# Optimization experiments

Measured on AMD Instinct MI355X. Metric: run time of the kernel, lower is better.

Reference implementation:

```python
import jax, jax.numpy as jnp
import numpy as np

N_NODES = 50000
E0, E1 = 500000, 300000
D = 64  # node_embedding_size == h_feats == edge_embedding_sizes[i]


def _mlp(x, w0, b0, w1, b1, w2, b2):
    # Linear -> ReLU -> Linear -> ReLU -> Linear (nodes_in / edges_in stacks)
    h = jax.nn.relu(x @ w0 + b0)
    h = jax.nn.relu(h @ w1 + b1)
    return h @ w2 + b2


def setup_inputs() -> dict:
    key = jax.random.key(0)
    ks = jax.random.split(key, 32)

    def lin(k, fi, fo):
        return (jax.random.uniform(k, (fi, fo), jnp.float32) - 0.5) * (2.0 / np.sqrt(fi))

    z = lambda n: jnp.zeros((n,), jnp.float32)
    inp = {}
    inp['node_feats'] = jax.random.normal(ks[0], (N_NODES, 32), jnp.float32)
    inp['edge_feats0'] = jax.random.normal(ks[1], (E0, 16), jnp.float32)
    inp['edge_feats1'] = jax.random.normal(ks[2], (E1, 8), jnp.float32)
    # nodes_in MLP
    inp['n_w0'], inp['n_b0'] = lin(ks[3], 32, D), z(D)
    inp['n_w1'], inp['n_b1'] = lin(ks[4], D, D), z(D)
    inp['n_w2'], inp['n_b2'] = lin(ks[5], D, D), z(D)
    # edges_in MLP for edge type 0 (16 -> 64)
    inp['e0_w0'], inp['e0_b0'] = lin(ks[6], 16, D), z(D)
    inp['e0_w1'], inp['e0_b1'] = lin(ks[7], D, D), z(D)
    inp['e0_w2'], inp['e0_b2'] = lin(ks[8], D, D), z(D)
    # edges_in MLP for edge type 1 (8 -> 64)
    inp['e1_w0'], inp['e1_b0'] = lin(ks[9], 8, D), z(D)
    inp['e1_w1'], inp['e1_b1'] = lin(ks[10], D, D), z(D)
    inp['e1_w2'], inp['e1_b2'] = lin(ks[11], D, D), z(D)
    # GraphConv weights
    inp['c1_w'], inp['c1_b'] = lin(ks[12], D, D), z(D)
    inp['c2_w'], inp['c2_b'] = lin(ks[13], D, 1), z(1)
    # edge list (type-0 edges first, then type-1 edges)
    inp['src'] = jax.random.randint(ks[14], (E0 + E1,), 0, N_NODES, dtype=jnp.int32)
    inp['dst'] = jax.random.randint(ks[15], (E0 + E1,), 0, N_NODES, dtype=jnp.int32)
    return inp


def reference(node_feats, edge_feats0, edge_feats1,
              n_w0, n_b0, n_w1, n_b1, n_w2, n_b2,
              e0_w0, e0_b0, e0_w1, e0_b1, e0_w2, e0_b2,
              e1_w0, e1_b0, e1_w1, e1_b1, e1_w2, e1_b2,
              c1_w, c1_b, c2_w, c2_b, src, dst):
    n = node_feats.shape[0]
    # dense embedding stacks
    hn = _mlp(node_feats, n_w0, n_b0, n_w1, n_b1, n_w2, n_b2)          # [N, D]
    he = jnp.concatenate([
        _mlp(edge_feats0, e0_w0, e0_b0, e0_w1, e0_b1, e0_w2, e0_b2),
        _mlp(edge_feats1, e1_w0, e1_b0, e1_w1, e1_b1, e1_w2, e1_b2),
    ], axis=0)                                                          # [E, D]
    # GraphConv symmetric normalization (DGL norm='both'), degrees clamped to 1
    ones = jnp.ones(src.shape, jnp.float32)
    deg_out = jnp.maximum(jax.ops.segment_sum(ones, src, num_segments=n), 1.0)
    deg_in = jnp.maximum(jax.ops.segment_sum(ones, dst, num_segments=n), 1.0)
    norm_e = jax.lax.rsqrt(deg_out[src] * deg_in[dst])[:, None]        # [E, 1]
    # conv1: u_add_v message plus edge embedding, normalized sum aggregation
    msg = (hn[src] + hn[dst] + he) * norm_e                            # [E, D]
    agg1 = jax.ops.segment_sum(msg, dst, num_segments=n)               # [N, D]
    h1 = jax.nn.relu(agg1 @ c1_w + c1_b)                               # [N, D]
    # conv2: standard GraphConv to scalar output
    agg2 = jax.ops.segment_sum(h1[src] * norm_e, dst, num_segments=n)  # [N, D]
    return agg2 @ c2_w + c2_b                                          # [N, 1]
```

## Files before the change

### kernel.cpp

```cpp
#include <hip/hip_runtime.h>

#define N_NODES 50000
#define NE0 500000
#define NE1 300000
#define NE (NE0 + NE1)
#define DD 64
#define ILV 9

typedef __bf16 bf16x8 __attribute__((ext_vector_type(8)));
typedef float f32x4 __attribute__((ext_vector_type(4)));
typedef unsigned short u16x8 __attribute__((ext_vector_type(8)));

__device__ __forceinline__ ushort f2bf(float x) {
  union { __bf16 h; ushort u; } v;
  v.h = (__bf16)x;
  return v.u;
}
__device__ __forceinline__ float bf2f(ushort u) {
  union { unsigned u; float f; } v;
  v.u = ((unsigned)u) << 16;
  return v.f;
}

__global__ void pack_k(const float* __restrict__ w00, const float* __restrict__ w01,
                       const float* __restrict__ w02, const float* __restrict__ w10,
                       const float* __restrict__ w11, const float* __restrict__ w12,
                       const float* __restrict__ w20, const float* __restrict__ w21,
                       const float* __restrict__ w22, ushort* __restrict__ pk) {
  int f = blockIdx.x, l = threadIdx.x;
  int t = f / 20, fl = f % 20;
  int layer, nt, ks;
  if (fl < 4) { layer = 0; nt = fl; ks = 0; }
  else if (fl < 12) { layer = 1; nt = (fl - 4) >> 1; ks = (fl - 4) & 1; }
  else { layer = 2; nt = (fl - 12) >> 1; ks = (fl - 12) & 1; }
  const float* Wt[3][3] = {{w00, w01, w02}, {w10, w11, w12}, {w20, w21, w22}};
  const int K0[3] = {16, 8, 32};
  const float* W = Wt[t][layer];
  int K = (layer == 0) ? K0[t] : 64;
  int g = l >> 4, c = l & 15;
  ushort o[8];
#pragma unroll
  for (int e = 0; e < 8; ++e) {
    int k = ks * 32 + g * 8 + e, n = nt * 16 + c;
    o[e] = f2bf((k < K) ? W[k * DD + n] : 0.f);
  }
  ushort4* d4 = (ushort4*)&pk[(size_t)f * 512 + l * 8];
  d4[0] = make_ushort4(o[0], o[1], o[2], o[3]);
  d4[1] = make_ushort4(o[4], o[5], o[6], o[7]);
}

__device__ __forceinline__ int block_scan_excl(int x, int tid, int* total) {
  int lane = tid & 63, w = tid >> 6;
  int incl = x;
#pragma unroll
  for (int d = 1; d < 64; d <<= 1) {
    int y = __shfl_up(incl, d);
    if (lane >= d) incl += y;
  }
  __shared__ int wsum[4];
  if (lane == 63) wsum[w] = incl;
  __syncthreads();
  int woff = 0;
  if (w > 0) woff = wsum[0];
  if (w > 1) woff += wsum[1];
  if (w > 2) woff += wsum[2];
  *total = wsum[0] + wsum[1] + wsum[2] + wsum[3];
  return woff + incl - x;
}

__global__ __launch_bounds__(256) void scan_k(const int* __restrict__ cnt,
                                              int* __restrict__ rowptr,
                                              int* __restrict__ gbase) {
  int i = blockIdx.x * 256 + threadIdx.x;
  int x = (i < N_NODES) ? cnt[i] : 0;
  int tot;
  int ex = block_scan_excl(x, threadIdx.x, &tot);
  __shared__ int base;
  if (threadIdx.x == 0) base = atomicAdd(gbase, tot);
  __syncthreads();
  if (i < N_NODES) rowptr[i] = base + ex;
}

__global__ void scatter_k(const int* __restrict__ src, const int* __restrict__ dst,
                          const int* __restrict__ rowptr,
                          const int* __restrict__ rank,
                          const int* __restrict__ cntO,
                          const int* __restrict__ cntI,
                          int4* __restrict__ cslot) {
  int e = blockIdx.x * 256 + threadIdx.x;
  if (e < NE) {
    int s = src[e], d = dst[e];
    int slot = rowptr[d] + rank[e];
    float nm = rsqrtf((float)max(cntO[s], 1) * (float)max(cntI[d], 1));
    int4 q;
    q.x = e;
    q.y = s;
    q.z = __float_as_int(nm);
    q.w = 0;
    cslot[slot] = q;
  }
}

template <int FIN, bool NODE>
__device__ __forceinline__ void mlp_body(
    ushort (*__restrict__ A)[72], const float* __restrict__ xin,
    const ushort* __restrict__ pk, int pkb, const float* __restrict__ B0,
    const float* __restrict__ B1, const float* __restrict__ B2,
    ushort* __restrict__ msg, float* __restrict__ hn, int r0w, int nR,
    int ebase) {
  const int l = threadIdx.x & 63;
  const int g = l >> 4, c = l & 15;

  {
    int row = l >> 1, half = l & 1;
    int r = r0w + row;
    bool ok = r < nR;
    if (FIN == 32) {
      int cq = half * 16;
#pragma unroll
      for (int q = 0; q < 4; ++q) {
        float4 v = make_float4(0.f, 0.f, 0.f, 0.f);
        if (ok) v = *(const float4*)(xin + (size_t)r * 32 + cq + q * 4);
        *(ushort4*)&A[row][cq + q * 4] =
            make_ushort4(f2bf(v.x), f2bf(v.y), f2bf(v.z), f2bf(v.w));
      }
    } else if (FIN == 16) {
      int cq = half * 8;
#pragma unroll
      for (int q = 0; q < 2; ++q) {
        float4 v = make_float4(0.f, 0.f, 0.f, 0.f);
        if (ok) v = *(const float4*)(xin + (size_t)r * 16 + cq + q * 4);
        *(ushort4*)&A[row][cq + q * 4] =
            make_ushort4(f2bf(v.x), f2bf(v.y), f2bf(v.z), f2bf(v.w));
      }
    } else {
      int cq = half * 4;
      float4 v = make_float4(0.f, 0.f, 0.f, 0.f);
      if (ok) v = *(const float4*)(xin + (size_t)r * 8 + cq);
      *(ushort4*)&A[row][cq] =
          make_ushort4(f2bf(v.x), f2bf(v.y), f2bf(v.z), f2bf(v.w));
    }
  }
  asm volatile("s_waitcnt lgkmcnt(0)" ::: "memory");

  f32x4 acc[2][4];
#pragma unroll
  for (int nt = 0; nt < 4; ++nt) {
    float b = B0[nt * 16 + c];
    acc[0][nt] = f32x4{b, b, b, b};
    acc[1][nt] = acc[0][nt];
  }
  {
    bf16x8 a0 = {}, a1 = {};
    if (g * 8 < FIN) {
      a0 = *(const bf16x8*)&A[c][g * 8];
      a1 = *(const bf16x8*)&A[16 + c][g * 8];
    }
#pragma unroll
    for (int nt = 0; nt < 4; ++nt) {
      bf16x8 bb = *(const bf16x8*)&pk[(size_t)(pkb + nt) * 512 + l * 8];
      acc[0][nt] = __builtin_amdgcn_mfma_f32_16x16x32_bf16(a0, bb, acc[0][nt], 0, 0, 0);
      acc[1][nt] = __builtin_amdgcn_mfma_f32_16x16x32_bf16(a1, bb, acc[1][nt], 0, 0, 0);
    }
  }
#pragma unroll
  for (int t = 0; t < 2; ++t)
#pragma unroll
    for (int nt = 0; nt < 4; ++nt)
#pragma unroll
      for (int r = 0; r < 4; ++r)
        A[t * 16 + g * 4 + r][nt * 16 + c] = f2bf(fmaxf(acc[t][nt][r], 0.f));
  asm volatile("s_waitcnt lgkmcnt(0)" ::: "memory");

#pragma unroll
  for (int nt = 0; nt < 4; ++nt) {
    float b = B1[nt * 16 + c];
    acc[0][nt] = f32x4{b, b, b, b};
    acc[1][nt] = acc[0][nt];
  }
  {
    bf16x8 x00 = *(const bf16x8*)&A[c][g * 8];
    bf16x8 x01 = *(const bf16x8*)&A[c][32 + g * 8];
    bf16x8 x10 = *(const bf16x8*)&A[16 + c][g * 8];
    bf16x8 x11 = *(const bf16x8*)&A[16 + c][32 + g * 8];
#pragma unroll
    for (int nt = 0; nt < 4; ++nt) {
      bf16x8 bb0 = *(const bf16x8*)&pk[(size_t)(pkb + 4 + nt * 2) * 512 + l * 8];
      bf16x8 bb1 = *(const bf16x8*)&pk[(size_t)(pkb + 5 + nt * 2) * 512 + l * 8];
      acc[0][nt] = __builtin_amdgcn_mfma_f32_16x16x32_bf16(x00, bb0, acc[0][nt], 0, 0, 0);
      acc[0][nt] = __builtin_amdgcn_mfma_f32_16x16x32_bf16(x01, bb1, acc[0][nt], 0, 0, 0);
      acc[1][nt] = __builtin_amdgcn_mfma_f32_16x16x32_bf16(x10, bb0, acc[1][nt], 0, 0, 0);
      acc[1][nt] = __builtin_amdgcn_mfma_f32_16x16x32_bf16(x11, bb1, acc[1][nt], 0, 0, 0);
    }
  }
#pragma unroll
  for (int t = 0; t < 2; ++t)
#pragma unroll
    for (int nt = 0; nt < 4; ++nt)
#pragma unroll
      for (int r = 0; r < 4; ++r)
        A[t * 16 + g * 4 + r][nt * 16 + c] = f2bf(fmaxf(acc[t][nt][r], 0.f));
  asm volatile("s_waitcnt lgkmcnt(0)" ::: "memory");

#pragma unroll
  for (int nt = 0; nt < 4; ++nt) {
    float b = B2[nt * 16 + c];
    acc[0][nt] = f32x4{b, b, b, b};
    acc[1][nt] = acc[0][nt];
  }
  {
    bf16x8 x00 = *(const bf16x8*)&A[c][g * 8];
    bf16x8 x01 = *(const bf16x8*)&A[c][32 + g * 8];
    bf16x8 x10 = *(const bf16x8*)&A[16 + c][g * 8];
    bf16x8 x11 = *(const bf16x8*)&A[16 + c][32 + g * 8];
#pragma unroll
    for (int nt = 0; nt < 4; ++nt) {
      bf16x8 bb0 = *(const bf16x8*)&pk[(size_t)(pkb + 12 + nt * 2) * 512 + l * 8];
      bf16x8 bb1 = *(const bf16x8*)&pk[(size_t)(pkb + 13 + nt * 2) * 512 + l * 8];
      acc[0][nt] = __builtin_amdgcn_mfma_f32_16x16x32_bf16(x00, bb0, acc[0][nt], 0, 0, 0);
      acc[0][nt] = __builtin_amdgcn_mfma_f32_16x16x32_bf16(x01, bb1, acc[0][nt], 0, 0, 0);
      acc[1][nt] = __builtin_amdgcn_mfma_f32_16x16x32_bf16(x10, bb0, acc[1][nt], 0, 0, 0);
      acc[1][nt] = __builtin_amdgcn_mfma_f32_16x16x32_bf16(x11, bb1, acc[1][nt], 0, 0, 0);
    }
  }

  if (NODE) {
#pragma unroll
    for (int t = 0; t < 2; ++t)
#pragma unroll
      for (int r = 0; r < 4; ++r) {
        int n = r0w + t * 16 + g * 4 + r;
        if (n < nR) {
          float* hp = hn + (size_t)n * DD + c;
#pragma unroll
          for (int nt = 0; nt < 4; ++nt) hp[nt * 16] = acc[t][nt][r];
        }
      }
  } else {
#pragma unroll
    for (int t = 0; t < 2; ++t)
#pragma unroll
      for (int nt = 0; nt < 4; ++nt)
#pragma unroll
        for (int r = 0; r < 4; ++r)
          A[t * 16 + g * 4 + r][nt * 16 + c] = f2bf(acc[t][nt][r]);
    asm volatile("s_waitcnt lgkmcnt(0)" ::: "memory");
#pragma unroll
    for (int p = 0; p < 4; ++p) {
      int row = p * 8 + (l >> 3);
      int col8 = (l & 7) * 8;
      u16x8 v = *(const u16x8*)&A[row][col8];
      if (r0w + row < nR)
        *(u16x8*)(msg + (size_t)(ebase + r0w + row) * DD + col8) = v;
    }
  }
}

__global__ __launch_bounds__(256, 6) void giant_k(
    const float* __restrict__ nf, const float* __restrict__ ef0,
    const float* __restrict__ ef1, const ushort* __restrict__ pk,
    const float* __restrict__ nb0, const float* __restrict__ nb1,
    const float* __restrict__ nb2, const float* __restrict__ b00,
    const float* __restrict__ b01, const float* __restrict__ b02,
    const float* __restrict__ b10, const float* __restrict__ b11,
    const float* __restrict__ b12, const int* __restrict__ src,
    const int* __restrict__ dst, int* __restrict__ cntO,
    int* __restrict__ cntI, int* __restrict__ rank,
    ushort* __restrict__ msg, float* __restrict__ hn,
    int NBc4, int NBn, int NB0v, int NB1v) {
  __shared__ __align__(16) ushort act[4][32][72];
  int bid = blockIdx.x, tid = threadIdx.x, wid = tid >> 6;
  int cnum = bid / ILV;
  if (bid % ILV == ILV - 1) {
    if (cnum < NBc4) {
      int t4 = (cnum * 256 + tid) * 4;
      if (t4 < NE) {
        int4 s4 = *(const int4*)(src + t4);
        int4 d4 = *(const int4*)(dst + t4);
        atomicAdd(cntO + s4.x, 1);
        atomicAdd(cntO + s4.y, 1);
        atomicAdd(cntO + s4.z, 1);
        atomicAdd(cntO + s4.w, 1);
        int4 r;
        r.x = atomicAdd(cntI + d4.x, 1);
        r.y = atomicAdd(cntI + d4.y, 1);
        r.z = atomicAdd(cntI + d4.z, 1);
        r.w = atomicAdd(cntI + d4.w, 1);
        *(int4*)(rank + t4) = r;
      }
    }
    return;
  }
  int mb = bid - cnum;
  if (mb >= NBn + NB0v + NB1v) return;
  ushort (*A)[72] = act[wid];
  if (mb < NBn) {
    mlp_body<32, true>(A, nf, pk, 40, nb0, nb1, nb2, nullptr, hn,
                       mb * 128 + wid * 32, N_NODES, 0);
  } else if (mb < NBn + NB0v) {
    mlp_body<16, false>(A, ef0, pk, 0, b00, b01, b02, msg, nullptr,
                        (mb - NBn) * 128 + wid * 32, NE0, 0);
  } else {
    mlp_body<8, false>(A, ef1, pk, 20, b10, b11, b12, msg, nullptr,
                       (mb - NBn - NB0v) * 128 + wid * 32, NE1, NE0);
  }
}

__global__ __launch_bounds__(256) void gather_conv1_k(
    const int* __restrict__ rowptr, const int* __restrict__ deg,
    const int4* __restrict__ cslot, const ushort* __restrict__ msgb,
    const float* __restrict__ hn, const float* __restrict__ c1w,
    const float* __restrict__ c1b, const float* __restrict__ c2w,
    float* __restrict__ sbuf) {
  int w = threadIdx.x >> 6, l = threadIdx.x & 63;
  int g = l >> 4, c = l & 15;
  int n = blockIdx.x * 4 + w;
  if (n >= N_NODES) return;
  int r0 = rowptr[n], r1 = r0 + deg[n];
  float a0 = 0.f, a1 = 0.f, a2 = 0.f, a3 = 0.f, sn = 0.f;
  for (int j0 = r0; j0 < r1; j0 += 16) {
#pragma unroll
    for (int u = 0; u < 4; ++u) {
      int j = j0 + u * 4 + g;
      bool v = j < r1;
      int js = v ? j : r0;
      int4 q = cslot[js];
      int e = q.x, s = q.y;
      float nm = v ? __int_as_float(q.z) : 0.f;
      ushort4 m = *(const ushort4*)(msgb + (size_t)e * DD + c * 4);
      float4 h = *(const float4*)(hn + (size_t)s * DD + c * 4);
      a0 = fmaf(nm, bf2f(m.x) + h.x, a0);
      a1 = fmaf(nm, bf2f(m.y) + h.y, a1);
      a2 = fmaf(nm, bf2f(m.z) + h.z, a2);
      a3 = fmaf(nm, bf2f(m.w) + h.w, a3);
      sn += nm;
    }
  }
  a0 += __shfl_xor(a0, 16); a0 += __shfl_xor(a0, 32);
  a1 += __shfl_xor(a1, 16); a1 += __shfl_xor(a1, 32);
  a2 += __shfl_xor(a2, 16); a2 += __shfl_xor(a2, 32);
  a3 += __shfl_xor(a3, 16); a3 += __shfl_xor(a3, 32);
  sn += __shfl_xor(sn, 16); sn += __shfl_xor(sn, 32);
  float4 hv = *(const float4*)(hn + (size_t)n * DD + c * 4);
  a0 = fmaf(sn, hv.x, a0);
  a1 = fmaf(sn, hv.y, a1);
  a2 = fmaf(sn, hv.z, a2);
  a3 = fmaf(sn, hv.w, a3);
  __shared__ float Asm[4][64];
  if (g == 0) *(float4*)&Asm[w][c * 4] = make_float4(a0, a1, a2, a3);
  float h = c1b[l];
#pragma unroll 8
  for (int k = 0; k < 64; ++k) h = fmaf(Asm[w][k], c1w[k * DD + l], h);
  h = fmaxf(h, 0.f);
  float v = h * c2w[l];
#pragma unroll
  for (int d = 32; d; d >>= 1) v += __shfl_xor(v, d);
  if (l == 0) sbuf[n] = v;
}

__global__ __launch_bounds__(256) void conv2_gather_k(
    const int* __restrict__ rowptr, const int* __restrict__ deg,
    const int4* __restrict__ cslot, const float* __restrict__ sbuf,
    const float* __restrict__ c2b, float* __restrict__ out) {
  int n = blockIdx.x * 16 + (threadIdx.x >> 4);
  int c = threadIdx.x & 15;
  if (n >= N_NODES) return;
  int r0 = rowptr[n], r1 = r0 + deg[n];
  float a = 0.f;
  for (int j = r0 + c; j < r1; j += 16) {
    int4 q = cslot[j];
    a = fmaf(__int_as_float(q.z), sbuf[q.y], a);
  }
  a += __shfl_xor(a, 1, 16);
  a += __shfl_xor(a, 2, 16);
  a += __shfl_xor(a, 4, 16);
  a += __shfl_xor(a, 8, 16);
  if (c == 0) out[n] = a + c2b[0];
}

extern "C" void kernel_launch(void* const* d_in, const int* in_sizes, int n_in,
                              void* d_out, int out_size, void* d_ws,
                              size_t ws_size, hipStream_t stream) {
  const float* nf   = (const float*)d_in[0];
  const float* ef0  = (const float*)d_in[1];
  const float* ef1  = (const float*)d_in[2];
  const float* n_w0 = (const float*)d_in[3];  const float* n_b0 = (const float*)d_in[4];
  const float* n_w1 = (const float*)d_in[5];  const float* n_b1 = (const float*)d_in[6];
  const float* n_w2 = (const float*)d_in[7];  const float* n_b2 = (const float*)d_in[8];
  const float* e0w0 = (const float*)d_in[9];  const float* e0b0 = (const float*)d_in[10];
  const float* e0w1 = (const float*)d_in[11]; const float* e0b1 = (const float*)d_in[12];
  const float* e0w2 = (const float*)d_in[13]; const float* e0b2 = (const float*)d_in[14];
  const float* e1w0 = (const float*)d_in[15]; const float* e1b0 = (const float*)d_in[16];
  const float* e1w1 = (const float*)d_in[17]; const float* e1b1 = (const float*)d_in[18];
  const float* e1w2 = (const float*)d_in[19]; const float* e1b2 = (const float*)d_in[20];
  const float* c1w  = (const float*)d_in[21]; const float* c1b  = (const float*)d_in[22];
  const float* c2w  = (const float*)d_in[23]; const float* c2b  = (const float*)d_in[24];
  const int* src = (const int*)d_in[25];
  const int* dst = (const int*)d_in[26];
  float* out = (float*)d_out;
  float* ws = (float*)d_ws;

  float*  hn     = ws;
  float*  sbuf   = ws + 3200000;
  int*    rowptr = (int*)(ws + 3250000);
  int*    cntI   = (int*)(ws + 3300008);
  int*    cntO   = (int*)(ws + 3350008);
  int*    gbase  = (int*)(ws + 3400008);
  int*    rank   = (int*)(ws + 3410000);
  int4*   cslot  = (int4*)(ws + 4210000);
  ushort* msg    = (ushort*)(ws + 7410000);
  ushort* pk     = (ushort*)(ws + 33010000);

  const int NB   = (N_NODES + 255) / 256;
  const int NBn  = (N_NODES + 127) / 128;
  const int NB0  = (NE0 + 127) / 128;
  const int NB1  = (NE1 + 127) / 128;
  const int NBc  = (NE + 255) / 256;
  const int NBc4 = (NE + 1023) / 1024;

  const int NMLP = NBn + NB0 + NB1;
  int T = NMLP + NBc4;
  while (T / ILV < NBc4 || T - T / ILV < NMLP) ++T;

  hipMemsetAsync(cntI, 0, (size_t)100016 * sizeof(int), stream);
  pack_k<<<60, 64, 0, stream>>>(e0w0, e0w1, e0w2, e1w0, e1w1, e1w2, n_w0,
                                n_w1, n_w2, pk);
  giant_k<<<T, 256, 0, stream>>>(
      nf, ef0, ef1, pk, n_b0, n_b1, n_b2, e0b0, e0b1, e0b2, e1b0, e1b1, e1b2,
      src, dst, cntO, cntI, rank, msg, hn, NBc4, NBn, NB0, NB1);
  scan_k<<<NB, 256, 0, stream>>>(cntI, rowptr, gbase);
  scatter_k<<<NBc, 256, 0, stream>>>(src, dst, rowptr, rank, cntO, cntI,
                                     cslot);
  gather_conv1_k<<<(N_NODES + 3) / 4, 256, 0, stream>>>(
      rowptr, cntI, cslot, msg, hn, c1w, c1b, c2w, sbuf);
  conv2_gather_k<<<(N_NODES + 15) / 16, 256, 0, stream>>>(
      rowptr, cntI, cslot, sbuf, c2b, out);
}
```

Measured before the change: 196.2 us.

## Fuse edge MLPs into per-node gather, dropping the bf16 edge message buffer

The edge-embedding MLP is no longer computed up front and written to a bf16 message buffer. It now runs inside the per-node gather kernel on 16-edge tiles read through the CSR slots, with the normalized results accumulated directly. In-degree counts are split by edge type so each node's type-0 and type-1 edges sit contiguously in CSR order and can use the matching MLP weights. The counting kernel now interleaves only the node MLP with the edge counting. This removes roughly 100MB of message write and reread traffic, but adds gathered, uncoalesced reads of edge features and partially filled MFMA tiles for low-degree nodes, which wastes MFMA work.

```diff
diff --git a/kernel.cpp b/kernel.cpp
--- a/kernel.cpp
+++ b/kernel.cpp
@@ -5,21 +5,14 @@
 #define NE1 300000
 #define NE (NE0 + NE1)
 #define DD 64
-#define ILV 9
 
 typedef __bf16 bf16x8 __attribute__((ext_vector_type(8)));
 typedef float f32x4 __attribute__((ext_vector_type(4)));
-typedef unsigned short u16x8 __attribute__((ext_vector_type(8)));
 
 __device__ __forceinline__ ushort f2bf(float x) {
   union { __bf16 h; ushort u; } v;
   v.h = (__bf16)x;
   return v.u;
-}
-__device__ __forceinline__ float bf2f(ushort u) {
-  union { unsigned u; float f; } v;
-  v.u = ((unsigned)u) << 16;
-  return v.f;
 }
 
 __global__ void pack_k(const float* __restrict__ w00, const float* __restrict__ w01,
@@ -68,11 +61,12 @@
   return woff + incl - x;
 }
 
-__global__ __launch_bounds__(256) void scan_k(const int* __restrict__ cnt,
+__global__ __launch_bounds__(256) void scan_k(const int* __restrict__ cntI0,
+                                              const int* __restrict__ cntI1,
                                               int* __restrict__ rowptr,
                                               int* __restrict__ gbase) {
   int i = blockIdx.x * 256 + threadIdx.x;
-  int x = (i < N_NODES) ? cnt[i] : 0;
+  int x = (i < N_NODES) ? (cntI0[i] + cntI1[i]) : 0;
   int tot;
   int ex = block_scan_excl(x, threadIdx.x, &tot);
   __shared__ int base;
@@ -85,13 +79,15 @@
                           const int* __restrict__ rowptr,
                           const int* __restrict__ rank,
                           const int* __restrict__ cntO,
-                          const int* __restrict__ cntI,
+                          const int* __restrict__ cntI0,
+                          const int* __restrict__ cntI1,
                           int4* __restrict__ cslot) {
   int e = blockIdx.x * 256 + threadIdx.x;
   if (e < NE) {
     int s = src[e], d = dst[e];
-    int slot = rowptr[d] + rank[e];
-    float nm = rsqrtf((float)max(cntO[s], 1) * (float)max(cntI[d], 1));
+    int slot = rowptr[d] + ((e < NE0) ? rank[e] : cntI0[d] + rank[e]);
+    float nm = rsqrtf((float)max(cntO[s], 1) *
+                      (float)max(cntI0[d] + cntI1[d], 1));
     int4 q;
     q.x = e;
     q.y = s;
@@ -101,48 +97,27 @@
   }
 }
 
-template <int FIN, bool NODE>
-__device__ __forceinline__ void mlp_body(
-    ushort (*__restrict__ A)[72], const float* __restrict__ xin,
-    const ushort* __restrict__ pk, int pkb, const float* __restrict__ B0,
+__device__ __forceinline__ void node_body(
+    ushort (*__restrict__ A)[72], const float* __restrict__ nf,
+    const ushort* __restrict__ pk, const float* __restrict__ B0,
     const float* __restrict__ B1, const float* __restrict__ B2,
-    ushort* __restrict__ msg, float* __restrict__ hn, int r0w, int nR,
-    int ebase) {
+    float* __restrict__ hn, int r0w) {
   const int l = threadIdx.x & 63;
   const int g = l >> 4, c = l & 15;
-
   {
     int row = l >> 1, half = l & 1;
     int r = r0w + row;
-    bool ok = r < nR;
-    if (FIN == 32) {
-      int cq = half * 16;
-#pragma unroll
-      for (int q = 0; q < 4; ++q) {
-        float4 v = make_float4(0.f, 0.f, 0.f, 0.f);
-        if (ok) v = *(const float4*)(xin + (size_t)r * 32 + cq + q * 4);
-        *(ushort4*)&A[row][cq + q * 4] =
-            make_ushort4(f2bf(v.x), f2bf(v.y), f2bf(v.z), f2bf(v.w));
-      }
-    } else if (FIN == 16) {
-      int cq = half * 8;
-#pragma unroll
-      for (int q = 0; q < 2; ++q) {
-        float4 v = make_float4(0.f, 0.f, 0.f, 0.f);
-        if (ok) v = *(const float4*)(xin + (size_t)r * 16 + cq + q * 4);
-        *(ushort4*)&A[row][cq + q * 4] =
-            make_ushort4(f2bf(v.x), f2bf(v.y), f2bf(v.z), f2bf(v.w));
-      }
-    } else {
-      int cq = half * 4;
+    bool ok = r < N_NODES;
+    int cq = half * 16;
+#pragma unroll
+    for (int q = 0; q < 4; ++q) {
       float4 v = make_float4(0.f, 0.f, 0.f, 0.f);
-      if (ok) v = *(const float4*)(xin + (size_t)r * 8 + cq);
-      *(ushort4*)&A[row][cq] =
+      if (ok) v = *(const float4*)(nf + (size_t)r * 32 + cq + q * 4);
+      *(ushort4*)&A[row][cq + q * 4] =
           make_ushort4(f2bf(v.x), f2bf(v.y), f2bf(v.z), f2bf(v.w));
     }
   }
   asm volatile("s_waitcnt lgkmcnt(0)" ::: "memory");
-
   f32x4 acc[2][4];
 #pragma unroll
   for (int nt = 0; nt < 4; ++nt) {
@@ -151,14 +126,11 @@
     acc[1][nt] = acc[0][nt];
   }
   {
-    bf16x8 a0 = {}, a1 = {};
-    if (g * 8 < FIN) {
-      a0 = *(const bf16x8*)&A[c][g * 8];
-      a1 = *(const bf16x8*)&A[16 + c][g * 8];
-    }
+    bf16x8 a0 = *(const bf16x8*)&A[c][g * 8];
+    bf16x8 a1 = *(const bf16x8*)&A[16 + c][g * 8];
 #pragma unroll
     for (int nt = 0; nt < 4; ++nt) {
-      bf16x8 bb = *(const bf16x8*)&pk[(size_t)(pkb + nt) * 512 + l * 8];
+      bf16x8 bb = *(const bf16x8*)&pk[(size_t)(40 + nt) * 512 + l * 8];
       acc[0][nt] = __builtin_amdgcn_mfma_f32_16x16x32_bf16(a0, bb, acc[0][nt], 0, 0, 0);
       acc[1][nt] = __builtin_amdgcn_mfma_f32_16x16x32_bf16(a1, bb, acc[1][nt], 0, 0, 0);
     }
@@ -171,109 +143,66 @@
       for (int r = 0; r < 4; ++r)
         A[t * 16 + g * 4 + r][nt * 16 + c] = f2bf(fmaxf(acc[t][nt][r], 0.f));
   asm volatile("s_waitcnt lgkmcnt(0)" ::: "memory");
-
-#pragma unroll
-  for (int nt = 0; nt < 4; ++nt) {
-    float b = B1[nt * 16 + c];
-    acc[0][nt] = f32x4{b, b, b, b};
-    acc[1][nt] = acc[0][nt];
-  }
-  {
+#pragma unroll
+  for (int L = 0; L < 2; ++L) {
+    const float* B = L ? B2 : B1;
+    int pb = L ? 52 : 44;
+#pragma unroll
+    for (int nt = 0; nt < 4; ++nt) {
+      float b = B[nt * 16 + c];
+      acc[0][nt] = f32x4{b, b, b, b};
+      acc[1][nt] = acc[0][nt];
+    }
     bf16x8 x00 = *(const bf16x8*)&A[c][g * 8];
     bf16x8 x01 = *(const bf16x8*)&A[c][32 + g * 8];
     bf16x8 x10 = *(const bf16x8*)&A[16 + c][g * 8];
     bf16x8 x11 = *(const bf16x8*)&A[16 + c][32 + g * 8];
 #pragma unroll
     for (int nt = 0; nt < 4; ++nt) {
-      bf16x8 bb0 = *(const bf16x8*)&pk[(size_t)(pkb + 4 + nt * 2) * 512 + l * 8];
-      bf16x8 bb1 = *(const bf16x8*)&pk[(size_t)(pkb + 5 + nt * 2) * 512 + l * 8];
+      bf16x8 bb0 = *(const bf16x8*)&pk[(size_t)(pb + nt * 2) * 512 + l * 8];
+      bf16x8 bb1 = *(const bf16x8*)&pk[(size_t)(pb + 1 + nt * 2) * 512 + l * 8];
       acc[0][nt] = __builtin_amdgcn_mfma_f32_16x16x32_bf16(x00, bb0, acc[0][nt], 0, 0, 0);
       acc[0][nt] = __builtin_amdgcn_mfma_f32_16x16x32_bf16(x01, bb1, acc[0][nt], 0, 0, 0);
       acc[1][nt] = __builtin_amdgcn_mfma_f32_16x16x32_bf16(x10, bb0, acc[1][nt], 0, 0, 0);
       acc[1][nt] = __builtin_amdgcn_mfma_f32_16x16x32_bf16(x11, bb1, acc[1][nt], 0, 0, 0);
     }
+    if (L == 0) {
+#pragma unroll
+      for (int t = 0; t < 2; ++t)
+#pragma unroll
+        for (int nt = 0; nt < 4; ++nt)
+#pragma unroll
+          for (int r = 0; r < 4; ++r)
+            A[t * 16 + g * 4 + r][nt * 16 + c] = f2bf(fmaxf(acc[t][nt][r], 0.f));
+      asm volatile("s_waitcnt lgkmcnt(0)" ::: "memory");
+    }
   }
 #pragma unroll
   for (int t = 0; t < 2; ++t)
 #pragma unroll
-    for (int nt = 0; nt < 4; ++nt)
-#pragma unroll
-      for (int r = 0; r < 4; ++r)
-        A[t * 16 + g * 4 + r][nt * 16 + c] = f2bf(fmaxf(acc[t][nt][r], 0.f));
-  asm volatile("s_waitcnt lgkmcnt(0)" ::: "memory");
-
-#pragma unroll
-  for (int nt = 0; nt < 4; ++nt) {
-    float b = B2[nt * 16 + c];
-    acc[0][nt] = f32x4{b, b, b, b};
-    acc[1][nt] = acc[0][nt];
-  }
-  {
-    bf16x8 x00 = *(const bf16x8*)&A[c][g * 8];
-    bf16x8 x01 = *(const bf16x8*)&A[c][32 + g * 8];
-    bf16x8 x10 = *(const bf16x8*)&A[16 + c][g * 8];
-    bf16x8 x11 = *(const bf16x8*)&A[16 + c][32 + g * 8];
-#pragma unroll
-    for (int nt = 0; nt < 4; ++nt) {
-      bf16x8 bb0 = *(const bf16x8*)&pk[(size_t)(pkb + 12 + nt * 2) * 512 + l * 8];
-      bf16x8 bb1 = *(const bf16x8*)&pk[(size_t)(pkb + 13 + nt * 2) * 512 + l * 8];
-      acc[0][nt] = __builtin_amdgcn_mfma_f32_16x16x32_bf16(x00, bb0, acc[0][nt], 0, 0, 0);
-      acc[0][nt] = __builtin_amdgcn_mfma_f32_16x16x32_bf16(x01, bb1, acc[0][nt], 0, 0, 0);
-      acc[1][nt] = __builtin_amdgcn_mfma_f32_16x16x32_bf16(x10, bb0, acc[1][nt], 0, 0, 0);
-      acc[1][nt] = __builtin_amdgcn_mfma_f32_16x16x32_bf16(x11, bb1, acc[1][nt], 0, 0, 0);
-    }
-  }
-
-  if (NODE) {
-#pragma unroll
-    for (int t = 0; t < 2; ++t)
-#pragma unroll
-      for (int r = 0; r < 4; ++r) {
-        int n = r0w + t * 16 + g * 4 + r;
-        if (n < nR) {
-          float* hp = hn + (size_t)n * DD + c;
-#pragma unroll
-          for (int nt = 0; nt < 4; ++nt) hp[nt * 16] = acc[t][nt][r];
-        }
+    for (int r = 0; r < 4; ++r) {
+      int n = r0w + t * 16 + g * 4 + r;
+      if (n < N_NODES) {
+        float* hp = hn + (size_t)n * DD + c;
+#pragma unroll
+        for (int nt = 0; nt < 4; ++nt) hp[nt * 16] = acc[t][nt][r];
       }
-  } else {
-#pragma unroll
-    for (int t = 0; t < 2; ++t)
-#pragma unroll
-      for (int nt = 0; nt < 4; ++nt)
-#pragma unroll
-        for (int r = 0; r < 4; ++r)
-          A[t * 16 + g * 4 + r][nt * 16 + c] = f2bf(acc[t][nt][r]);
-    asm volatile("s_waitcnt lgkmcnt(0)" ::: "memory");
-#pragma unroll
-    for (int p = 0; p < 4; ++p) {
-      int row = p * 8 + (l >> 3);
-      int col8 = (l & 7) * 8;
-      u16x8 v = *(const u16x8*)&A[row][col8];
-      if (r0w + row < nR)
-        *(u16x8*)(msg + (size_t)(ebase + r0w + row) * DD + col8) = v;
-    }
-  }
-}
-
-__global__ __launch_bounds__(256, 6) void giant_k(
-    const float* __restrict__ nf, const float* __restrict__ ef0,
-    const float* __restrict__ ef1, const ushort* __restrict__ pk,
+    }
+}
+
+__global__ __launch_bounds__(256, 6) void countnode_k(
+    const float* __restrict__ nf, const ushort* __restrict__ pk,
     const float* __restrict__ nb0, const float* __restrict__ nb1,
-    const float* __restrict__ nb2, const float* __restrict__ b00,
-    const float* __restrict__ b01, const float* __restrict__ b02,
-    const float* __restrict__ b10, const float* __restrict__ b11,
-    const float* __restrict__ b12, const int* __restrict__ src,
+    const float* __restrict__ nb2, const int* __restrict__ src,
     const int* __restrict__ dst, int* __restrict__ cntO,
-    int* __restrict__ cntI, int* __restrict__ rank,
-    ushort* __restrict__ msg, float* __restrict__ hn,
-    int NBc4, int NBn, int NB0v, int NB1v) {
+    int* __restrict__ cntI0, int* __restrict__ cntI1,
+    int* __restrict__ rank, float* __restrict__ hn, int NBc4, int NBn) {
   __shared__ __align__(16) ushort act[4][32][72];
   int bid = blockIdx.x, tid = threadIdx.x, wid = tid >> 6;
-  int cnum = bid / ILV;
-  if (bid % ILV == ILV - 1) {
-    if (cnum < NBc4) {
-      int t4 = (cnum * 256 + tid) * 4;
+  if (bid % 3 != 2) {
+    int cidx = (bid / 3) * 2 + (bid % 3);
+    if (cidx < NBc4) {
+      int t4 = (cidx * 256 + tid) * 4;
       if (t4 < NE) {
         int4 s4 = *(const int4*)(src + t4);
         int4 d4 = *(const int4*)(dst + t4);
@@ -281,58 +210,155 @@
         atomicAdd(cntO + s4.y, 1);
         atomicAdd(cntO + s4.z, 1);
         atomicAdd(cntO + s4.w, 1);
+        int* cI = (t4 < NE0) ? cntI0 : cntI1;
         int4 r;
-        r.x = atomicAdd(cntI + d4.x, 1);
-        r.y = atomicAdd(cntI + d4.y, 1);
-        r.z = atomicAdd(cntI + d4.z, 1);
-        r.w = atomicAdd(cntI + d4.w, 1);
+        r.x = atomicAdd(cI + d4.x, 1);
+        r.y = atomicAdd(cI + d4.y, 1);
+        r.z = atomicAdd(cI + d4.z, 1);
+        r.w = atomicAdd(cI + d4.w, 1);
         *(int4*)(rank + t4) = r;
       }
     }
     return;
   }
-  int mb = bid - cnum;
-  if (mb >= NBn + NB0v + NB1v) return;
-  ushort (*A)[72] = act[wid];
-  if (mb < NBn) {
-    mlp_body<32, true>(A, nf, pk, 40, nb0, nb1, nb2, nullptr, hn,
-                       mb * 128 + wid * 32, N_NODES, 0);
-  } else if (mb < NBn + NB0v) {
-    mlp_body<16, false>(A, ef0, pk, 0, b00, b01, b02, msg, nullptr,
-                        (mb - NBn) * 128 + wid * 32, NE0, 0);
-  } else {
-    mlp_body<8, false>(A, ef1, pk, 20, b10, b11, b12, msg, nullptr,
-                       (mb - NBn - NB0v) * 128 + wid * 32, NE1, NE0);
-  }
-}
-
-__global__ __launch_bounds__(256) void gather_conv1_k(
-    const int* __restrict__ rowptr, const int* __restrict__ deg,
-    const int4* __restrict__ cslot, const ushort* __restrict__ msgb,
-    const float* __restrict__ hn, const float* __restrict__ c1w,
-    const float* __restrict__ c1b, const float* __restrict__ c2w,
-    float* __restrict__ sbuf) {
+  int nb = bid / 3;
+  if (nb >= NBn) return;
+  node_body(act[wid], nf, pk, nb0, nb1, nb2, hn, nb * 128 + wid * 32);
+}
+
+template <int FIN>
+__device__ __forceinline__ void mlp_tile(
+    ushort (*__restrict__ A)[72], const int4* __restrict__ cslot, int js,
+    int dgc, const float* __restrict__ ef, const ushort* __restrict__ pk,
+    int pkb, const float* __restrict__ B0, const float* __restrict__ B1,
+    const float* __restrict__ B2, float* __restrict__ psum, int l, int g,
+    int c, int esub) {
+  bool vm = c < dgc;
+  int4 q = make_int4(0, 0, 0, 0);
+  if (vm) q = cslot[js + c];
+  float nmv = vm ? __int_as_float(q.z) : 0.f;
+  bf16x8 a = {};
+  if (vm && g * 8 < FIN) {
+    const float* rp = ef + (size_t)(q.x - esub) * FIN + g * 8;
+    float4 v0 = *(const float4*)rp;
+    float4 v1 = *(const float4*)(rp + 4);
+    a[0] = (__bf16)v0.x; a[1] = (__bf16)v0.y;
+    a[2] = (__bf16)v0.z; a[3] = (__bf16)v0.w;
+    a[4] = (__bf16)v1.x; a[5] = (__bf16)v1.y;
+    a[6] = (__bf16)v1.z; a[7] = (__bf16)v1.w;
+  }
+  f32x4 acc[4];
+#pragma unroll
+  for (int nt = 0; nt < 4; ++nt) {
+    float b = B0[nt * 16 + c];
+    acc[nt] = f32x4{b, b, b, b};
+  }
+#pragma unroll
+  for (int nt = 0; nt < 4; ++nt) {
+    bf16x8 bb = *(const bf16x8*)&pk[(size_t)(pkb + nt) * 512 + l * 8];
+    acc[nt] = __builtin_amdgcn_mfma_f32_16x16x32_bf16(a, bb, acc[nt], 0, 0, 0);
+  }
+#pragma unroll
+  for (int nt = 0; nt < 4; ++nt)
+#pragma unroll
+    for (int r = 0; r < 4; ++r)
+      A[g * 4 + r][nt * 16 + c] = f2bf(fmaxf(acc[nt][r], 0.f));
+  asm volatile("s_waitcnt lgkmcnt(0)" ::: "memory");
+#pragma unroll
+  for (int nt = 0; nt < 4; ++nt) {
+    float b = B1[nt * 16 + c];
+    acc[nt] = f32x4{b, b, b, b};
+  }
+  {
+    bf16x8 x0 = *(const bf16x8*)&A[c][g * 8];
+    bf16x8 x1 = *(const bf16x8*)&A[c][32 + g * 8];
+#pragma unroll
+    for (int nt = 0; nt < 4; ++nt) {
+      bf16x8 bb0 = *(const bf16x8*)&pk[(size_t)(pkb + 4 + nt * 2) * 512 + l * 8];
+      bf16x8 bb1 = *(const bf16x8*)&pk[(size_t)(pkb + 5 + nt * 2) * 512 + l * 8];
+      acc[nt] = __builtin_amdgcn_mfma_f32_16x16x32_bf16(x0, bb0, acc[nt], 0, 0, 0);
+      acc[nt] = __builtin_amdgcn_mfma_f32_16x16x32_bf16(x1, bb1, acc[nt], 0, 0, 0);
+    }
+  }
+#pragma unroll
+  for (int nt = 0; nt < 4; ++nt)
+#pragma unroll
+    for (int r = 0; r < 4; ++r)
+      A[g * 4 + r][nt * 16 + c] = f2bf(fmaxf(acc[nt][r], 0.f));
+  asm volatile("s_waitcnt lgkmcnt(0)" ::: "memory");
+#pragma unroll
+  for (int nt = 0; nt < 4; ++nt) {
+    float b = B2[nt * 16 + c];
+    acc[nt] = f32x4{b, b, b, b};
+  }
+  {
+    bf16x8 x0 = *(const bf16x8*)&A[c][g * 8];
+    bf16x8 x1 = *(const bf16x8*)&A[c][32 + g * 8];
+#pragma unroll
+    for (int nt = 0; nt < 4; ++nt) {
+      bf16x8 bb0 = *(const bf16x8*)&pk[(size_t)(pkb + 12 + nt * 2) * 512 + l * 8];
+      bf16x8 bb1 = *(const bf16x8*)&pk[(size_t)(pkb + 13 + nt * 2) * 512 + l * 8];
+      acc[nt] = __builtin_amdgcn_mfma_f32_16x16x32_bf16(x0, bb0, acc[nt], 0, 0, 0);
+      acc[nt] = __builtin_amdgcn_mfma_f32_16x16x32_bf16(x1, bb1, acc[nt], 0, 0, 0);
+    }
+  }
+  float nm0 = __shfl(nmv, g * 4 + 0);
+  float nm1 = __shfl(nmv, g * 4 + 1);
+  float nm2 = __shfl(nmv, g * 4 + 2);
+  float nm3 = __shfl(nmv, g * 4 + 3);
+#pragma unroll
+  for (int nt = 0; nt < 4; ++nt) {
+    psum[nt] = fmaf(nm0, acc[nt][0], psum[nt]);
+    psum[nt] = fmaf(nm1, acc[nt][1], psum[nt]);
+    psum[nt] = fmaf(nm2, acc[nt][2], psum[nt]);
+    psum[nt] = fmaf(nm3, acc[nt][3], psum[nt]);
+  }
+}
+
+__global__ __launch_bounds__(256) void gather_mega_k(
+    const int* __restrict__ rowptr, const int* __restrict__ cntI0,
+    const int* __restrict__ cntI1, const int4* __restrict__ cslot,
+    const float* __restrict__ ef0, const float* __restrict__ ef1,
+    const ushort* __restrict__ pk, const float* __restrict__ b00,
+    const float* __restrict__ b01, const float* __restrict__ b02,
+    const float* __restrict__ b10, const float* __restrict__ b11,
+    const float* __restrict__ b12, const float* __restrict__ hn,
+    const float* __restrict__ c1w, const float* __restrict__ c1b,
+    const float* __restrict__ c2w, float* __restrict__ sbuf) {
+  __shared__ __align__(16) ushort At[4][16][72];
+  __shared__ float Asm[4][64];
   int w = threadIdx.x >> 6, l = threadIdx.x & 63;
   int g = l >> 4, c = l & 15;
   int n = blockIdx.x * 4 + w;
   if (n >= N_NODES) return;
-  int r0 = rowptr[n], r1 = r0 + deg[n];
+  int r0 = rowptr[n], d0 = cntI0[n], d1 = cntI1[n];
+  int r1 = r0 + d0 + d1;
+  float psum[4] = {0.f, 0.f, 0.f, 0.f};
+  for (int js = r0; js < r0 + d0; js += 16)
+    mlp_tile<16>(At[w], cslot, js, min(16, r0 + d0 - js), ef0, pk, 0, b00,
+                 b01, b02, psum, l, g, c, 0);
+  for (int js = r0 + d0; js < r1; js += 16)
+    mlp_tile<8>(At[w], cslot, js, min(16, r1 - js), ef1, pk, 20, b10, b11,
+                b12, psum, l, g, c, NE0);
+#pragma unroll
+  for (int nt = 0; nt < 4; ++nt) {
+    psum[nt] += __shfl_xor(psum[nt], 16);
+    psum[nt] += __shfl_xor(psum[nt], 32);
+  }
   float a0 = 0.f, a1 = 0.f, a2 = 0.f, a3 = 0.f, sn = 0.f;
   for (int j0 = r0; j0 < r1; j0 += 16) {
 #pragma unroll
     for (int u = 0; u < 4; ++u) {
       int j = j0 + u * 4 + g;
       bool v = j < r1;
-      int js = v ? j : r0;
-      int4 q = cslot[js];
-      int e = q.x, s = q.y;
+      int js_ = v ? j : r0;
+      int4 q = cslot[js_];
       float nm = v ? __int_as_float(q.z) : 0.f;
-      ushort4 m = *(const ushort4*)(msgb + (size_t)e * DD + c * 4);
-      float4 h = *(const float4*)(hn + (size_t)s * DD + c * 4);
-      a0 = fmaf(nm, bf2f(m.x) + h.x, a0);
-      a1 = fmaf(nm, bf2f(m.y) + h.y, a1);
-      a2 = fmaf(nm, bf2f(m.z) + h.z, a2);
-      a3 = fmaf(nm, bf2f(m.w) + h.w, a3);
+      float4 h = *(const float4*)(hn + (size_t)q.y * DD + c * 4);
+      a0 = fmaf(nm, h.x, a0);
+      a1 = fmaf(nm, h.y, a1);
+      a2 = fmaf(nm, h.z, a2);
+      a3 = fmaf(nm, h.w, a3);
       sn += nm;
     }
   }
@@ -346,8 +372,13 @@
   a1 = fmaf(sn, hv.y, a1);
   a2 = fmaf(sn, hv.z, a2);
   a3 = fmaf(sn, hv.w, a3);
-  __shared__ float Asm[4][64];
   if (g == 0) *(float4*)&Asm[w][c * 4] = make_float4(a0, a1, a2, a3);
+  asm volatile("s_waitcnt lgkmcnt(0)" ::: "memory");
+  if (g == 0) {
+#pragma unroll
+    for (int nt = 0; nt < 4; ++nt) Asm[w][nt * 16 + c] += psum[nt];
+  }
+  asm volatile("s_waitcnt lgkmcnt(0)" ::: "memory");
   float h = c1b[l];
 #pragma unroll 8
   for (int k = 0; k < 64; ++k) h = fmaf(Asm[w][k], c1w[k * DD + l], h);
@@ -359,13 +390,14 @@
 }
 
 __global__ __launch_bounds__(256) void conv2_gather_k(
-    const int* __restrict__ rowptr, const int* __restrict__ deg,
-    const int4* __restrict__ cslot, const float* __restrict__ sbuf,
-    const float* __restrict__ c2b, float* __restrict__ out) {
+    const int* __restrict__ rowptr, const int* __restrict__ cntI0,
+    const int* __restrict__ cntI1, const int4* __restrict__ cslot,
+    const float* __restrict__ sbuf, const float* __restrict__ c2b,
+    float* __restrict__ out) {
   int n = blockIdx.x * 16 + (threadIdx.x >> 4);
   int c = threadIdx.x & 15;
   if (n >= N_NODES) return;
-  int r0 = rowptr[n], r1 = r0 + deg[n];
+  int r0 = rowptr[n], r1 = r0 + cntI0[n] + cntI1[n];
   float a = 0.f;
   for (int j = r0 + c; j < r1; j += 16) {
     int4 q = cslot[j];
@@ -403,36 +435,31 @@
   float*  hn     = ws;
   float*  sbuf   = ws + 3200000;
   int*    rowptr = (int*)(ws + 3250000);
-  int*    cntI   = (int*)(ws + 3300008);
-  int*    cntO   = (int*)(ws + 3350008);
-  int*    gbase  = (int*)(ws + 3400008);
-  int*    rank   = (int*)(ws + 3410000);
-  int4*   cslot  = (int4*)(ws + 4210000);
-  ushort* msg    = (ushort*)(ws + 7410000);
-  ushort* pk     = (ushort*)(ws + 33010000);
+  int*    cntI0  = (int*)(ws + 3300000);
+  int*    cntI1  = (int*)(ws + 3350000);
+  int*    cntO   = (int*)(ws + 3400000);
+  int*    gbase  = (int*)(ws + 3450000);
+  int*    rank   = (int*)(ws + 3460000);
+  int4*   cslot  = (int4*)(ws + 4260000);
+  ushort* pk     = (ushort*)(ws + 7460000);
 
   const int NB   = (N_NODES + 255) / 256;
   const int NBn  = (N_NODES + 127) / 128;
-  const int NB0  = (NE0 + 127) / 128;
-  const int NB1  = (NE1 + 127) / 128;
   const int NBc  = (NE + 255) / 256;
   const int NBc4 = (NE + 1023) / 1024;
-
-  const int NMLP = NBn + NB0 + NB1;
-  int T = NMLP + NBc4;
-  while (T / ILV < NBc4 || T - T / ILV < NMLP) ++T;
-
-  hipMemsetAsync(cntI, 0, (size_t)100016 * sizeof(int), stream);
+  const int T = 3 * NBn;
+
+  hipMemsetAsync(cntI0, 0, (size_t)150016 * sizeof(int), stream);
   pack_k<<<60, 64, 0, stream>>>(e0w0, e0w1, e0w2, e1w0, e1w1, e1w2, n_w0,
                                 n_w1, n_w2, pk);
-  giant_k<<<T, 256, 0, stream>>>(
-      nf, ef0, ef1, pk, n_b0, n_b1, n_b2, e0b0, e0b1, e0b2, e1b0, e1b1, e1b2,
-      src, dst, cntO, cntI, rank, msg, hn, NBc4, NBn, NB0, NB1);
-  scan_k<<<NB, 256, 0, stream>>>(cntI, rowptr, gbase);
-  scatter_k<<<NBc, 256, 0, stream>>>(src, dst, rowptr, rank, cntO, cntI,
-                                     cslot);
-  gather_conv1_k<<<(N_NODES + 3) / 4, 256, 0, stream>>>(
-      rowptr, cntI, cslot, msg, hn, c1w, c1b, c2w, sbuf);
+  countnode_k<<<T, 256, 0, stream>>>(nf, pk, n_b0, n_b1, n_b2, src, dst,
+                                     cntO, cntI0, cntI1, rank, hn, NBc4, NBn);
+  scan_k<<<NB, 256, 0, stream>>>(cntI0, cntI1, rowptr, gbase);
+  scatter_k<<<NBc, 256, 0, stream>>>(src, dst, rowptr, rank, cntO, cntI0,
+                                     cntI1, cslot);
+  gather_mega_k<<<(N_NODES + 3) / 4, 256, 0, stream>>>(
+      rowptr, cntI0, cntI1, cslot, ef0, ef1, pk, e0b0, e0b1, e0b2, e1b0,
+      e1b1, e1b2, hn, c1w, c1b, c2w, sbuf);
   conv2_gather_k<<<(N_NODES + 15) / 16, 256, 0, stream>>>(
-      rowptr, cntI, cslot, sbuf, c2b, out);
-}
+      rowptr, cntI0, cntI1, cslot, sbuf, c2b, out);
+}
```

New measurement: 327.0 us. +66.6%, slower.
